# Kernel optimization log

Measured on AMD Instinct MI355X. Metric: run time of the kernel, lower is better.

## Reference

```python
import jax, jax.numpy as jnp
import numpy as np

CHUNK = 1024  # rows of pc0 processed per tile to avoid materializing the full NxM matrix


def _min_sqdist(a, b):
    """For each row of a [N,3], min squared distance to rows of b [M,3]."""
    b_sq = jnp.sum(b * b, axis=1)  # [M]

    def tile_min(ac):  # ac: [CHUNK, 3]
        d = jnp.sum(ac * ac, axis=1)[:, None] + b_sq[None, :] - 2.0 * (ac @ b.T)
        return jnp.min(d, axis=1)

    n, dim = a.shape
    return jax.lax.map(tile_min, a.reshape(n // CHUNK, CHUNK, dim)).reshape(n)


def setup_inputs() -> dict:
    key = jax.random.key(0)
    k0, k1 = jax.random.split(key)
    pc0 = jax.random.normal(k0, (65536, 3), dtype=jnp.float32)
    pc1 = jax.random.normal(k1, (65536, 3), dtype=jnp.float32)
    return {"pc0": pc0, "pc1": pc1}


def reference(pc0, pc1):
    # chamfer forward: dist0[i] = min_j ||pc0[i]-pc1[j]||^2
    dist0 = _min_sqdist(pc0, pc1)
    mask = dist0 <= 2.0
    # mean over selected elements (boolean mask is constant wrt grads, as in torch)
    return jnp.sum(jnp.where(mask, dist0, 0.0)) / jnp.sum(mask).astype(dist0.dtype)
```

## Files before the change

### kernel.cpp

```cpp
#include <hip/hip_runtime.h>


constexpr int   NPTS  = 65536;
constexpr int   G     = 64;
constexpr int   NC    = G * G * G;
constexpr float H     = 0.125f;
constexpr float ORG   = -4.0f;
constexpr float INVH  = 8.0f;
constexpr int   G3    = 32;
constexpr float H3    = 0.25f;
constexpr float INVH3 = 4.0f;
constexpr int   BLOCK = 256;
constexpr int   PBLOCKS = 1024;
constexpr int   SB    = 128;
constexpr int   CHUNK = NC / SB;

__device__ __forceinline__ int cellOf(float x) {
  int c = (int)floorf((x - ORG) * INVH);
  return min(max(c, 0), G - 1);
}
__device__ __forceinline__ int cellOf3(float x) {
  int c = (int)floorf((x - ORG) * INVH3);
  return min(max(c, 0), G3 - 1);
}

__global__ __launch_bounds__(BLOCK) void count_kernel(
    const float* __restrict__ pc0, const float* __restrict__ pc1,
    unsigned* __restrict__ counts0, unsigned* __restrict__ counts1) {
  const int gid = blockIdx.x * BLOCK + threadIdx.x;
  const float* p; unsigned* cnt; int i;
  if (gid < NPTS) { p = pc1; cnt = counts1; i = gid; }
  else            { p = pc0; cnt = counts0; i = gid - NPTS; }
  const float x = p[3 * i], y = p[3 * i + 1], z = p[3 * i + 2];
  atomicAdd(&cnt[(cellOf(z) * G + cellOf(y)) * G + cellOf(x)], 1u);
}

__global__ __launch_bounds__(1024) void scan_partial_kernel(
    const unsigned* __restrict__ counts0, const unsigned* __restrict__ counts1,
    unsigned* __restrict__ partials) {
  const unsigned* counts = blockIdx.y ? counts0 : counts1;
  const int base = blockIdx.x * CHUNK + threadIdx.x * 2;
  unsigned sum = counts[base] + counts[base + 1];
  for (int o = 32; o; o >>= 1) sum += __shfl_down(sum, o, 64);
  __shared__ unsigned ws[16];
  if ((threadIdx.x & 63) == 0) ws[threadIdx.x >> 6] = sum;
  __syncthreads();
  if (threadIdx.x == 0) {
    unsigned t = 0;
    for (int w = 0; w < 16; ++w) t += ws[w];
    partials[blockIdx.y * SB + blockIdx.x] = t;
  }
}

__global__ __launch_bounds__(256) void scan_mid_kernel(
    unsigned* __restrict__ partials) {
  const int tid = threadIdx.x;
  const int g   = tid >> 7;
  const int li  = tid & 127;
  const unsigned v = partials[g * SB + li];
  unsigned inc = v;
  for (int o = 1; o < 64; o <<= 1) {
    const unsigned t = __shfl_up(inc, o, 64);
    if ((tid & 63) >= o) inc += t;
  }
  __shared__ unsigned wt[4];
  if ((tid & 63) == 63) wt[tid >> 6] = inc;
  __syncthreads();
  const unsigned woff = ((tid >> 6) & 1) ? wt[g << 1] : 0u;
  partials[g * SB + li] = woff + inc - v;
}

__global__ __launch_bounds__(1024) void scan_final_kernel(
    const unsigned* __restrict__ counts0, unsigned* __restrict__ cur0,
    const unsigned* __restrict__ counts1, unsigned* __restrict__ cur1,
    const unsigned* __restrict__ partials) {
  const unsigned* counts = blockIdx.y ? counts0 : counts1;
  unsigned* cur          = blockIdx.y ? cur0    : cur1;
  const int tid = threadIdx.x;
  const int base = blockIdx.x * CHUNK + tid * 2;
  const unsigned a = counts[base], b = counts[base + 1];
  const unsigned tsum = a + b;
  unsigned inc = tsum;
  for (int o = 1; o < 64; o <<= 1) {
    const unsigned t = __shfl_up(inc, o, 64);
    if ((tid & 63) >= o) inc += t;
  }
  __shared__ unsigned wt[16];
  if ((tid & 63) == 63) wt[tid >> 6] = inc;
  __syncthreads();
  if (tid < 16) {
    unsigned w = wt[tid];
    for (int o = 1; o < 16; o <<= 1) {
      const unsigned t = __shfl_up(w, o, 16);
      if (tid >= o) w += t;
    }
    wt[tid] = w;
  }
  __syncthreads();
  const unsigned woff = (tid >> 6) ? wt[(tid >> 6) - 1] : 0u;
  const unsigned off =
      partials[blockIdx.y * SB + blockIdx.x] + woff + inc - tsum;
  cur[base] = off;
  cur[base + 1] = off + a;
}

__global__ __launch_bounds__(BLOCK) void scatter_kernel(
    const float* __restrict__ pc0, const float* __restrict__ pc1,
    unsigned* __restrict__ cur0, unsigned* __restrict__ cur1,
    float4* __restrict__ q, float4* __restrict__ s) {
  const int gid = blockIdx.x * BLOCK + threadIdx.x;
  const float* p; unsigned* cur; float4* dst; int i;
  if (gid < NPTS) { p = pc1; cur = cur1; dst = s; i = gid; }
  else            { p = pc0; cur = cur0; dst = q; i = gid - NPTS; }
  const float x = p[3 * i], y = p[3 * i + 1], z = p[3 * i + 2];
  const int cid = (cellOf(z) * G + cellOf(y)) * G + cellOf(x);
  dst[atomicAdd(&cur[cid], 1u)] = make_float4(x, y, z, 0.f);
}

__global__ __launch_bounds__(BLOCK) void query_kernel(
    const float4* __restrict__ q, const unsigned* __restrict__ ends,
    const float4* __restrict__ s,
    unsigned* __restrict__ wl, float* __restrict__ wlBest,
    unsigned* __restrict__ pendCnt, float* __restrict__ bkt) {
  const int gtid = blockIdx.x * BLOCK + threadIdx.x;
  const int i   = gtid >> 1;
  const int sub = gtid & 1;
  const float4 p = q[i];
  const int cx = cellOf(p.x), cy = cellOf(p.y), cz = cellOf(p.z);
  const int x0 = max(cx - 1, 0), x1 = min(cx + 1, G - 1);

  unsigned rs[9], re[9];
#pragma unroll
  for (int rr = 0; rr < 9; ++rr) {
    const int zz = cz + rr / 3 - 1, yy = cy + rr % 3 - 1;
    const bool ok = (zz >= 0) && (zz < G) && (yy >= 0) && (yy < G);
    const int rb = ok ? (zz * G + yy) * G : 0;
    rs[rr] = ok ? ((rb + x0) ? ends[rb + x0 - 1] : 0u) : 0u;
    re[rr] = ok ? ends[rb + x1] : 0u;
  }
  float best = 3.4e38f;
#pragma unroll
  for (int rr = 0; rr < 9; ++rr) {
#pragma unroll 4
    for (unsigned j = rs[rr] + sub; j < re[rr]; j += 2) {
      const float4 c = s[j];
      const float dx = p.x - c.x, dy = p.y - c.y, dz = p.z - c.z;
      best = fminf(best, fmaf(dx, dx, fmaf(dy, dy, dz * dz)));
    }
  }
  best = fminf(best, __shfl_xor(best, 1, 64));

  float v = 0.f, c = 0.f;
  if (sub == 0) {
    if (best > H * H) {
      const unsigned k = atomicAdd(pendCnt, 1u);
      wl[k] = (unsigned)i; wlBest[k] = best;
    } else if (best <= 2.0f) { v = best; c = 1.0f; }
  }

  for (int o = 32; o; o >>= 1) {
    v += __shfl_down(v, o, 64);
    c += __shfl_down(c, o, 64);
  }
  __shared__ float wsum[BLOCK / 64], wcnt[BLOCK / 64];
  const int wid = threadIdx.x >> 6;
  if ((threadIdx.x & 63) == 0) { wsum[wid] = v; wcnt[wid] = c; }
  __syncthreads();
  if (threadIdx.x == 0) {
    float bv = 0.f, bc = 0.f;
    for (int w = 0; w < BLOCK / 64; ++w) { bv += wsum[w]; bc += wcnt[w]; }
    if (bc != 0.f) {
      atomicAdd(&bkt[2 * (blockIdx.x & 63) + 0], bv);
      atomicAdd(&bkt[2 * (blockIdx.x & 63) + 1], bc);
    }
  }
}

__global__ __launch_bounds__(BLOCK) void pending_kernel(
    const float4* __restrict__ q,
    const unsigned* __restrict__ ends, const float4* __restrict__ s,
    const unsigned* __restrict__ wl, const float* __restrict__ wlBest,
    unsigned* __restrict__ pendCnt, float* __restrict__ bkt,
    unsigned* __restrict__ done, float* __restrict__ out) {
  __shared__ int snP;
  __shared__ float wsum[BLOCK / 64], wcnt[BLOCK / 64];
  __shared__ int isLast;
  __shared__ float fs[BLOCK / 64], fc[BLOCK / 64];
  if (threadIdx.x == 0) snP = (int)atomicAdd(pendCnt, 0u);
  __syncthreads();
  const int lane = threadIdx.x & 63, wid = threadIdx.x >> 6;
  const int gw = blockIdx.x * (BLOCK / 64) + wid;
  const int nW = PBLOCKS * (BLOCK / 64);
  float v = 0.f, c = 0.f;

  for (int it = gw; it < snP; it += nW) {
    const unsigned qi = wl[it];
    const float4 p = q[qi];
    const int cx = cellOf3(p.x), cy = cellOf3(p.y), cz = cellOf3(p.z);
    float best = wlBest[it];

    for (int r = 1; r <= 8; ++r) {
      const float cov = H3 * (float)(r - 1);
      if (best <= cov * cov) break;
      if (best > 2.0f && cov * cov >= 2.0f) break;
      const int S = (r == 1) ? 9 : 8 * r + 2 * (2 * r - 1) * (2 * r - 1);
      float b = best;
      for (int sI = lane; sI < S; sI += 64) {
        int dz, dy, xa, xb;
        if (r == 1) {
          dz = sI / 3 - 1; dy = sI % 3 - 1; xa = cx - 1; xb = cx + 1;
        } else if (sI < 8 * r) {
          if (sI < 2 * r + 1)      { dz = -r; dy = sI - r; }
          else if (sI < 4 * r + 2) { dz =  r; dy = sI - (2 * r + 1) - r; }
          else { const int t2 = sI - (4 * r + 2); dz = (t2 >> 1) - (r - 1);
                 dy = (t2 & 1) ? r : -r; }
          xa = cx - r; xb = cx + r;
        } else {
          const int t2 = sI - 8 * r, ci = t2 >> 1, w1 = 2 * r - 1;
          dz = ci / w1 - (r - 1); dy = ci % w1 - (r - 1);
          xa = xb = (t2 & 1) ? cx + r : cx - r;
        }
        const int Z = cz + dz, Y = cy + dy;
        if (Z < 0 || Z >= G3 || Y < 0 || Y >= G3) continue;
        const int a3 = max(xa, 0), e3 = min(xb, G3 - 1);
        if (a3 > e3) continue;
        const int xs = 2 * a3, xe = 2 * e3 + 1;
        unsigned js[4], je[4];
#pragma unroll
        for (int k = 0; k < 4; ++k) {
          const int zz = 2 * Z + (k >> 1), yy = 2 * Y + (k & 1);
          const int rb = (zz * G + yy) * G;
          js[k] = (rb + xs) ? ends[rb + xs - 1] : 0u;
          je[k] = ends[rb + xe];
        }
#pragma unroll
        for (int k = 0; k < 4; ++k) {
#pragma unroll 4
          for (unsigned j = js[k]; j < je[k]; ++j) {
            const float4 cd = s[j];
            const float dx = p.x - cd.x, dyv = p.y - cd.y, dzv = p.z - cd.z;
            b = fminf(b, fmaf(dx, dx, fmaf(dyv, dyv, dzv * dzv)));
          }
        }
      }
      for (int o = 32; o; o >>= 1) b = fminf(b, __shfl_xor(b, o, 64));
      best = b;
    }
    if (lane == 0 && best <= 2.0f) { v += best; c += 1.0f; }
  }

  if (lane == 0) { wsum[wid] = v; wcnt[wid] = c; }
  __syncthreads();
  if (threadIdx.x == 0) {
    float bv = 0.f, bc = 0.f;
    for (int w = 0; w < BLOCK / 64; ++w) { bv += wsum[w]; bc += wcnt[w]; }
    if (bc != 0.f) {
      atomicAdd(&bkt[2 * (blockIdx.x & 63) + 0], bv);
      atomicAdd(&bkt[2 * (blockIdx.x & 63) + 1], bc);
    }
    __threadfence();
    isLast = (atomicAdd(done, 1u) == (unsigned)(PBLOCKS - 1));
  }
  __syncthreads();
  if (isLast) {
    const float val = (threadIdx.x < 128) ? atomicAdd(&bkt[threadIdx.x], 0.0f) : 0.0f;
    float sv = (threadIdx.x & 1) ? 0.f : val;
    float cv = (threadIdx.x & 1) ? val : 0.f;
    for (int o = 32; o; o >>= 1) {
      sv += __shfl_down(sv, o, 64);
      cv += __shfl_down(cv, o, 64);
    }
    if (lane == 0) { fs[wid] = sv; fc[wid] = cv; }
    __syncthreads();
    if (threadIdx.x == 0) {
      float S = 0.f, C = 0.f;
      for (int w = 0; w < BLOCK / 64; ++w) { S += fs[w]; C += fc[w]; }
      out[0] = S / C;
    }
  }
}

extern "C" void kernel_launch(void* const* d_in, const int* in_sizes, int n_in,
                              void* d_out, int out_size, void* d_ws, size_t ws_size,
                              hipStream_t stream) {
  const float* pc0 = (const float*)d_in[0];
  const float* pc1 = (const float*)d_in[1];
  float* out = (float*)d_out;

  char* w = (char*)d_ws;
  auto nxt = [&](size_t bytes) {
    char* p = w; w += (bytes + 255) & ~(size_t)255; return p;
  };
  unsigned* counts1  = (unsigned*)nxt((size_t)NC * 4);
  unsigned* counts0  = (unsigned*)nxt((size_t)NC * 4);
  char*     misc     = nxt(1024);
  float*    bkt      = (float*)misc;
  unsigned* done     = (unsigned*)(misc + 512);
  unsigned* pendCnt  = (unsigned*)(misc + 516);
  unsigned* partials = (unsigned*)nxt((size_t)2 * SB * 4);
  unsigned* cur1     = (unsigned*)nxt((size_t)NC * 4);
  unsigned* cur0     = (unsigned*)nxt((size_t)NC * 4);
  float4*   s        = (float4*)nxt((size_t)NPTS * 16);
  float4*   q        = (float4*)nxt((size_t)NPTS * 16);
  unsigned* wl       = (unsigned*)nxt((size_t)NPTS * 4);
  float*    wlBest   = (float*)nxt((size_t)NPTS * 4);

  hipMemsetAsync(counts1, 0, (size_t)2 * NC * 4 + 1024, stream);

  count_kernel<<<2 * NPTS / BLOCK, BLOCK, 0, stream>>>(pc0, pc1, counts0, counts1);
  scan_partial_kernel<<<dim3(SB, 2), 1024, 0, stream>>>(counts0, counts1, partials);
  scan_mid_kernel<<<1, 256, 0, stream>>>(partials);
  scan_final_kernel<<<dim3(SB, 2), 1024, 0, stream>>>(counts0, cur0,
                                                      counts1, cur1, partials);
  scatter_kernel<<<2 * NPTS / BLOCK, BLOCK, 0, stream>>>(
      pc0, pc1, cur0, cur1, q, s);
  query_kernel<<<2 * NPTS / BLOCK, BLOCK, 0, stream>>>(q, cur1, s, wl, wlBest,
                                                       pendCnt, bkt);
  pending_kernel<<<PBLOCKS, BLOCK, 0, stream>>>(q, cur1, s, wl, wlBest,
                                                pendCnt, bkt, done, out);
}
```

Baseline: 149.7 us.

## Cap ring search at radius two and brute-force leftover deep queries

The pending kernel now stops its expanding shell search after radius 2. Queries whose best distance is still above the covered radius are pushed to a second worklist. A new deep kernel gives each such query one block and scans all 65536 target points exhaustively, then does the final reduction. This removes the long divergent tail of wide-radius searches in exchange for a full O(M) scan per outlier query plus an extra kernel launch.

```diff
diff --git a/kernel.cpp b/kernel.cpp
--- a/kernel.cpp
+++ b/kernel.cpp
@@ -12,6 +12,7 @@
 constexpr float INVH3 = 4.0f;
 constexpr int   BLOCK = 256;
 constexpr int   PBLOCKS = 1024;
+constexpr int   DBLOCKS = 512;
 constexpr int   SB    = 128;
 constexpr int   CHUNK = NC / SB;
 
@@ -181,11 +182,9 @@
     const unsigned* __restrict__ ends, const float4* __restrict__ s,
     const unsigned* __restrict__ wl, const float* __restrict__ wlBest,
     unsigned* __restrict__ pendCnt, float* __restrict__ bkt,
-    unsigned* __restrict__ done, float* __restrict__ out) {
+    unsigned* __restrict__ wl2, unsigned* __restrict__ deepCnt) {
   __shared__ int snP;
   __shared__ float wsum[BLOCK / 64], wcnt[BLOCK / 64];
-  __shared__ int isLast;
-  __shared__ float fs[BLOCK / 64], fc[BLOCK / 64];
   if (threadIdx.x == 0) snP = (int)atomicAdd(pendCnt, 0u);
   __syncthreads();
   const int lane = threadIdx.x & 63, wid = threadIdx.x >> 6;
@@ -199,26 +198,25 @@
     const int cx = cellOf3(p.x), cy = cellOf3(p.y), cz = cellOf3(p.z);
     float best = wlBest[it];
 
-    for (int r = 1; r <= 8; ++r) {
+    for (int r = 1; r <= 2; ++r) {
       const float cov = H3 * (float)(r - 1);
       if (best <= cov * cov) break;
-      if (best > 2.0f && cov * cov >= 2.0f) break;
-      const int S = (r == 1) ? 9 : 8 * r + 2 * (2 * r - 1) * (2 * r - 1);
+      const int S = (r == 1) ? 9 : 34;
       float b = best;
       for (int sI = lane; sI < S; sI += 64) {
         int dz, dy, xa, xb;
         if (r == 1) {
           dz = sI / 3 - 1; dy = sI % 3 - 1; xa = cx - 1; xb = cx + 1;
-        } else if (sI < 8 * r) {
-          if (sI < 2 * r + 1)      { dz = -r; dy = sI - r; }
-          else if (sI < 4 * r + 2) { dz =  r; dy = sI - (2 * r + 1) - r; }
-          else { const int t2 = sI - (4 * r + 2); dz = (t2 >> 1) - (r - 1);
-                 dy = (t2 & 1) ? r : -r; }
-          xa = cx - r; xb = cx + r;
+        } else if (sI < 16) {
+          if (sI < 5)       { dz = -2; dy = sI - 2; }
+          else if (sI < 10) { dz =  2; dy = sI - 5 - 2; }
+          else { const int t2 = sI - 10; dz = (t2 >> 1) - 1;
+                 dy = (t2 & 1) ? 2 : -2; }
+          xa = cx - 2; xb = cx + 2;
         } else {
-          const int t2 = sI - 8 * r, ci = t2 >> 1, w1 = 2 * r - 1;
-          dz = ci / w1 - (r - 1); dy = ci % w1 - (r - 1);
-          xa = xb = (t2 & 1) ? cx + r : cx - r;
+          const int t2 = sI - 16, ci = t2 >> 1;
+          dz = ci / 3 - 1; dy = ci % 3 - 1;
+          xa = xb = (t2 & 1) ? cx + 2 : cx - 2;
         }
         const int Z = cz + dz, Y = cy + dy;
         if (Z < 0 || Z >= G3 || Y < 0 || Y >= G3) continue;
@@ -246,7 +244,12 @@
       for (int o = 32; o; o >>= 1) b = fminf(b, __shfl_xor(b, o, 64));
       best = b;
     }
-    if (lane == 0 && best <= 2.0f) { v += best; c += 1.0f; }
+
+    if (lane == 0) {
+      if (best > 0.25f) {
+        wl2[atomicAdd(deepCnt, 1u)] = qi;
+      } else if (best <= 2.0f) { v += best; c += 1.0f; }
+    }
   }
 
   if (lane == 0) { wsum[wid] = v; wcnt[wid] = c; }
@@ -258,8 +261,51 @@
       atomicAdd(&bkt[2 * (blockIdx.x & 63) + 0], bv);
       atomicAdd(&bkt[2 * (blockIdx.x & 63) + 1], bc);
     }
+  }
+}
+
+__global__ __launch_bounds__(BLOCK) void deep_kernel(
+    const float4* __restrict__ q, const float4* __restrict__ s,
+    const unsigned* __restrict__ wl2, unsigned* __restrict__ deepCnt,
+    float* __restrict__ bkt, unsigned* __restrict__ done,
+    float* __restrict__ out) {
+  __shared__ int snD;
+  __shared__ float wmin[BLOCK / 64];
+  __shared__ float wsum[BLOCK / 64], wcnt[BLOCK / 64];
+  __shared__ int isLast;
+  __shared__ float fs[BLOCK / 64], fc[BLOCK / 64];
+  if (threadIdx.x == 0) snD = (int)atomicAdd(deepCnt, 0u);
+  __syncthreads();
+  const int lane = threadIdx.x & 63, wid = threadIdx.x >> 6;
+  float v = 0.f, c = 0.f;
+
+  for (int it = blockIdx.x; it < snD; it += DBLOCKS) {
+    const float4 p = q[wl2[it]];
+    float best = 3.4e38f;
+#pragma unroll 4
+    for (int j = threadIdx.x; j < NPTS; j += BLOCK) {
+      const float4 cd = s[j];
+      const float dx = p.x - cd.x, dy = p.y - cd.y, dz = p.z - cd.z;
+      best = fminf(best, fmaf(dx, dx, fmaf(dy, dy, dz * dz)));
+    }
+    for (int o = 32; o; o >>= 1) best = fminf(best, __shfl_xor(best, o, 64));
+    if (lane == 0) wmin[wid] = best;
+    __syncthreads();
+    if (threadIdx.x == 0) {
+      float b = wmin[0];
+      for (int w = 1; w < BLOCK / 64; ++w) b = fminf(b, wmin[w]);
+      if (b <= 2.0f) { v += b; c += 1.0f; }
+    }
+    __syncthreads();
+  }
+
+  if (threadIdx.x == 0) {
+    if (c != 0.f) {
+      atomicAdd(&bkt[2 * (blockIdx.x & 63) + 0], v);
+      atomicAdd(&bkt[2 * (blockIdx.x & 63) + 1], c);
+    }
     __threadfence();
-    isLast = (atomicAdd(done, 1u) == (unsigned)(PBLOCKS - 1));
+    isLast = (atomicAdd(done, 1u) == (unsigned)(DBLOCKS - 1));
   }
   __syncthreads();
   if (isLast) {
@@ -297,6 +343,7 @@
   float*    bkt      = (float*)misc;
   unsigned* done     = (unsigned*)(misc + 512);
   unsigned* pendCnt  = (unsigned*)(misc + 516);
+  unsigned* deepCnt  = (unsigned*)(misc + 520);
   unsigned* partials = (unsigned*)nxt((size_t)2 * SB * 4);
   unsigned* cur1     = (unsigned*)nxt((size_t)NC * 4);
   unsigned* cur0     = (unsigned*)nxt((size_t)NC * 4);
@@ -304,6 +351,7 @@
   float4*   q        = (float4*)nxt((size_t)NPTS * 16);
   unsigned* wl       = (unsigned*)nxt((size_t)NPTS * 4);
   float*    wlBest   = (float*)nxt((size_t)NPTS * 4);
+  unsigned* wl2      = (unsigned*)nxt((size_t)NPTS * 4);
 
   hipMemsetAsync(counts1, 0, (size_t)2 * NC * 4 + 1024, stream);
 
@@ -317,5 +365,6 @@
   query_kernel<<<2 * NPTS / BLOCK, BLOCK, 0, stream>>>(q, cur1, s, wl, wlBest,
                                                        pendCnt, bkt);
   pending_kernel<<<PBLOCKS, BLOCK, 0, stream>>>(q, cur1, s, wl, wlBest,
-                                                pendCnt, bkt, done, out);
-}
+                                                pendCnt, bkt, wl2, deepCnt);
+  deep_kernel<<<DBLOCKS, BLOCK, 0, stream>>>(q, s, wl2, deepCnt, bkt, done, out);
+}
```

After: 179.7 us. 1.2x slower.
